# Performance work log

Hardware: AMD Instinct MI355X
Metric: run time of the kernel (lower is better)

The kernel has to match this reference:

```python
import jax, jax.numpy as jnp
import numpy as np

N = 100000
IN_DIM = 512
OUT_DIM = 512


def setup_inputs() -> dict:
    key = jax.random.key(0)
    k1, k2, k3, k4 = jax.random.split(key, 4)
    x = jax.random.normal(k1, (N, IN_DIM), dtype=jnp.float32)
    edge_index = jax.random.randint(k2, (2, N), 0, N, dtype=jnp.int64)
    # Linear params (torch nn.Linear: out = x @ W.T + b)
    bound = 1.0 / np.sqrt(IN_DIM)
    W = jax.random.uniform(k3, (OUT_DIM, IN_DIM), minval=-bound, maxval=bound, dtype=jnp.float32)
    b = jax.random.uniform(k4, (OUT_DIM,), minval=-bound, maxval=bound, dtype=jnp.float32)
    return {"x": x, "edge_index": edge_index, "W": W, "b": b}


def reference(x, edge_index, W, b):
    # out = relu(linear(x))
    out = jax.nn.relu(jnp.einsum('ni,oi->no', x, W) + b)  # [N, OUT_DIM]
    # torch.scatter_add(out, 0, col[:, None], x):
    # index has shape [E, 1] so only column 0 of src (= x) is scattered:
    # out[col[e], 0] += x[e, 0]
    col = edge_index[1].astype(jnp.int32)  # [E], E == N here
    E = col.shape[0]
    out = out.at[col, 0].add(x[:E, 0])
    return out
```

## Files before the change

### kernel.cpp

```cpp
#include <hip/hip_runtime.h>
#include <stdint.h>

#define K_DIM 512
#define N_OUT 512
#define BM 128
#define BN 128
#define BK 64

typedef __bf16 bf16x8 __attribute__((ext_vector_type(8)));
typedef float f32x4 __attribute__((ext_vector_type(4)));
typedef unsigned short ushort8 __attribute__((ext_vector_type(8)));

__device__ inline unsigned short f2bf(float f) {
  unsigned u = __float_as_uint(f);
  u += 0x7fffu + ((u >> 16) & 1u);
  return (unsigned short)(u >> 16);
}

__global__ __launch_bounds__(256) void cvt_bf16_kernel(const float* __restrict__ src,
                                                       unsigned short* __restrict__ dst,
                                                       int n8) {
  int i = blockIdx.x * 256 + threadIdx.x;
  if (i >= n8) return;
  const float4* s = (const float4*)src + (size_t)i * 2;
  float4 a = s[0], c = s[1];
  ushort8 o;
  o[0] = f2bf(a.x); o[1] = f2bf(a.y); o[2] = f2bf(a.z); o[3] = f2bf(a.w);
  o[4] = f2bf(c.x); o[5] = f2bf(c.y); o[6] = f2bf(c.z); o[7] = f2bf(c.w);
  *(ushort8*)(dst + (size_t)i * 8) = o;
}

__global__ __launch_bounds__(256) void gemm_bf16_kernel(
    const unsigned short* __restrict__ xb, const unsigned short* __restrict__ wb,
    const float* __restrict__ b, float* __restrict__ out, int M) {
  __shared__ __align__(16) unsigned short Als[BM * BK];
  __shared__ __align__(16) unsigned short Bls[BN * BK];

  const int tid = threadIdx.x;
  const int lane = tid & 63;
  const int quad = lane >> 4;
  const int l16 = lane & 15;
  const int waveId = tid >> 6;
  const int wm = (waveId >> 1) * 64;
  const int wn = (waveId & 1) * 64;
  const int blockM = blockIdx.y * BM;
  const int blockN = blockIdx.x * BN;

  size_t goffA[4], goffB[4];
  int ldsoff[4];
#pragma unroll
  for (int i = 0; i < 4; ++i) {
    int ch = i * 256 + tid;
    int row = ch >> 3;
    int c8 = ch & 7;
    int sc = c8 ^ (row & 7);
    int ga_row = blockM + row;
    if (ga_row > M - 1) ga_row = M - 1;
    goffA[i] = (size_t)ga_row * K_DIM + sc * 8;
    goffB[i] = (size_t)(blockN + row) * K_DIM + sc * 8;
    ldsoff[i] = ch * 8;
  }

  f32x4 acc[4][4] = {};

  for (int k0 = 0; k0 < K_DIM; k0 += BK) {
#pragma unroll
    for (int i = 0; i < 4; ++i) {
      __builtin_amdgcn_global_load_lds(
          (const __attribute__((address_space(1))) void*)(xb + goffA[i] + k0),
          (__attribute__((address_space(3))) void*)(&Als[ldsoff[i]]), 16, 0, 0);
      __builtin_amdgcn_global_load_lds(
          (const __attribute__((address_space(1))) void*)(wb + goffB[i] + k0),
          (__attribute__((address_space(3))) void*)(&Bls[ldsoff[i]]), 16, 0, 0);
    }
    __syncthreads();

#pragma unroll
    for (int s = 0; s < 2; ++s) {
      bf16x8 af[4], bfr[4];
#pragma unroll
      for (int mi = 0; mi < 4; ++mi) {
        int r = wm + mi * 16 + l16;
        int c = (s * 4 + quad) ^ (r & 7);
        af[mi] = *(const bf16x8*)(&Als[r * BK + c * 8]);
      }
#pragma unroll
      for (int ni = 0; ni < 4; ++ni) {
        int r = wn + ni * 16 + l16;
        int c = (s * 4 + quad) ^ (r & 7);
        bfr[ni] = *(const bf16x8*)(&Bls[r * BK + c * 8]);
      }
#pragma unroll
      for (int mi = 0; mi < 4; ++mi)
#pragma unroll
        for (int ni = 0; ni < 4; ++ni)
          acc[mi][ni] = __builtin_amdgcn_mfma_f32_16x16x32_bf16(af[mi], bfr[ni], acc[mi][ni], 0, 0, 0);
    }
    __syncthreads();
  }

#pragma unroll
  for (int ni = 0; ni < 4; ++ni) {
    int gcol = blockN + wn + ni * 16 + l16;
    float bias = b[gcol];
#pragma unroll
    for (int mi = 0; mi < 4; ++mi) {
#pragma unroll
      for (int r = 0; r < 4; ++r) {
        int grow = blockM + wm + mi * 16 + quad * 4 + r;
        if (grow < M) {
          float v = acc[mi][ni][r] + bias;
          out[(size_t)grow * N_OUT + gcol] = v > 0.f ? v : 0.f;
        }
      }
    }
  }
}

#define LDS_STRIDE 40
__global__ __launch_bounds__(256) void gemm_fused_kernel(
    const float* __restrict__ x, const float* __restrict__ W,
    const float* __restrict__ b, float* __restrict__ out, int M) {
  __shared__ __align__(16) unsigned short Als[BM * LDS_STRIDE];
  __shared__ __align__(16) unsigned short Bls[BN * LDS_STRIDE];
  const int tid = threadIdx.x;
  const int lane = tid & 63;
  const int quad = lane >> 4;
  const int l16 = lane & 15;
  const int waveId = tid >> 6;
  const int wm = (waveId >> 1) * 64;
  const int wn = (waveId & 1) * 64;
  const int blockM = blockIdx.y * BM;
  const int blockN = blockIdx.x * BN;
  f32x4 acc[4][4] = {};
  for (int k0 = 0; k0 < K_DIM; k0 += 32) {
#pragma unroll
    for (int i = 0; i < 4; ++i) {
      int idx = i * 256 + tid;
      int row = idx >> 3;
      int c4 = idx & 7;
      float4 va = make_float4(0.f, 0.f, 0.f, 0.f);
      int grow = blockM + row;
      if (grow < M) va = *(const float4*)(x + (size_t)grow * K_DIM + k0 + c4 * 4);
      ushort4 ha;
      ha.x = f2bf(va.x); ha.y = f2bf(va.y); ha.z = f2bf(va.z); ha.w = f2bf(va.w);
      *(ushort4*)(&Als[row * LDS_STRIDE + c4 * 4]) = ha;
      float4 vb = *(const float4*)(W + (size_t)(blockN + row) * K_DIM + k0 + c4 * 4);
      ushort4 hb;
      hb.x = f2bf(vb.x); hb.y = f2bf(vb.y); hb.z = f2bf(vb.z); hb.w = f2bf(vb.w);
      *(ushort4*)(&Bls[row * LDS_STRIDE + c4 * 4]) = hb;
    }
    __syncthreads();
    bf16x8 af[4], bfr[4];
#pragma unroll
    for (int mi = 0; mi < 4; ++mi)
      af[mi] = *(const bf16x8*)(&Als[(wm + mi * 16 + l16) * LDS_STRIDE + quad * 8]);
#pragma unroll
    for (int ni = 0; ni < 4; ++ni)
      bfr[ni] = *(const bf16x8*)(&Bls[(wn + ni * 16 + l16) * LDS_STRIDE + quad * 8]);
#pragma unroll
    for (int mi = 0; mi < 4; ++mi)
#pragma unroll
      for (int ni = 0; ni < 4; ++ni)
        acc[mi][ni] = __builtin_amdgcn_mfma_f32_16x16x32_bf16(af[mi], bfr[ni], acc[mi][ni], 0, 0, 0);
    __syncthreads();
  }
#pragma unroll
  for (int ni = 0; ni < 4; ++ni) {
    int gcol = blockN + wn + ni * 16 + l16;
    float bias = b[gcol];
#pragma unroll
    for (int mi = 0; mi < 4; ++mi) {
#pragma unroll
      for (int r = 0; r < 4; ++r) {
        int grow = blockM + wm + mi * 16 + quad * 4 + r;
        if (grow < M) {
          float v = acc[mi][ni][r] + bias;
          out[(size_t)grow * N_OUT + gcol] = v > 0.f ? v : 0.f;
        }
      }
    }
  }
}

__global__ void scatter_kernel(const float* __restrict__ x,
                               const int* __restrict__ ei,
                               float* __restrict__ out, int E) {
  int e = blockIdx.x * 256 + threadIdx.x;
  if (e < E) {
    int c = ei[E + e];
    atomicAdd(out + (size_t)c * N_OUT, x[(size_t)e * K_DIM]);
  }
}

extern "C" void kernel_launch(void* const* d_in, const int* in_sizes, int n_in,
                              void* d_out, int out_size, void* d_ws, size_t ws_size,
                              hipStream_t stream) {
  const float* x = (const float*)d_in[0];
  const int* ei = (const int*)d_in[1];
  const float* W = (const float*)d_in[2];
  const float* b = (const float*)d_in[3];
  float* out = (float*)d_out;

  int M = in_sizes[0] / K_DIM;
  int E = in_sizes[1] / 2;

  size_t x_elems = (size_t)M * K_DIM;
  size_t w_elems = (size_t)N_OUT * K_DIM;
  size_t need = (x_elems + w_elems) * 2;

  dim3 grid(N_OUT / BN, (M + BM - 1) / BM);

  if (ws_size >= need) {
    unsigned short* xb = (unsigned short*)d_ws;
    unsigned short* wb = xb + x_elems;
    int n8x = (int)(x_elems / 8);
    int n8w = (int)(w_elems / 8);
    cvt_bf16_kernel<<<(n8x + 255) / 256, 256, 0, stream>>>(x, xb, n8x);
    cvt_bf16_kernel<<<(n8w + 255) / 256, 256, 0, stream>>>(W, wb, n8w);
    gemm_bf16_kernel<<<grid, 256, 0, stream>>>(xb, wb, b, out, M);
  } else {
    gemm_fused_kernel<<<grid, 256, 0, stream>>>(x, W, b, out, M);
  }
  scatter_kernel<<<(E + 255) / 256, 256, 0, stream>>>(x, ei, out, E);
}
```

Before: 496.6 us.

## Fuse x bf16 conversion into GEMM and pre-scatter column zero into buffer

Drops the separate full-matrix fp32-to-bf16 conversion of x. The GEMM now loads fp32 x directly, converts it in registers and writes it to LDS, while W still arrives through the direct global-to-LDS path. The scatter now accumulates into a small per-row buffer that the GEMM epilogue adds to column 0, which removes the atomic read-modify-write pass over the output. The change also adds XCD-aware workgroup remapping and nontemporal output stores. The cost is that the x loads now go through registers, with no async direct-to-LDS copy for A, which adds register pressure and VALU conversion work inside the main loop.

```diff
diff --git a/kernel.cpp b/kernel.cpp
--- a/kernel.cpp
+++ b/kernel.cpp
@@ -30,9 +30,25 @@
   *(ushort8*)(dst + (size_t)i * 8) = o;
 }
 
-__global__ __launch_bounds__(256) void gemm_bf16_kernel(
-    const unsigned short* __restrict__ xb, const unsigned short* __restrict__ wb,
-    const float* __restrict__ b, float* __restrict__ out, int M) {
+__global__ __launch_bounds__(256) void zero_f32_kernel(float* __restrict__ p, int n) {
+  int i = blockIdx.x * 256 + threadIdx.x;
+  if (i < n) p[i] = 0.f;
+}
+
+__global__ __launch_bounds__(256) void scatter_s_kernel(const float* __restrict__ x,
+                                                        const int* __restrict__ ei,
+                                                        float* __restrict__ s, int E) {
+  int e = blockIdx.x * 256 + threadIdx.x;
+  if (e < E) {
+    int c = ei[E + e];
+    atomicAdd(s + c, x[(size_t)e * K_DIM]);
+  }
+}
+
+__global__ __launch_bounds__(256) void gemm_fused2_kernel(
+    const float* __restrict__ x, const unsigned short* __restrict__ wb,
+    const float* __restrict__ b, const float* __restrict__ s,
+    float* __restrict__ out, int M) {
   __shared__ __align__(16) unsigned short Als[BM * BK];
   __shared__ __align__(16) unsigned short Bls[BN * BK];
 
@@ -43,8 +59,14 @@
   const int waveId = tid >> 6;
   const int wm = (waveId >> 1) * 64;
   const int wn = (waveId & 1) * 64;
-  const int blockM = blockIdx.y * BM;
-  const int blockN = blockIdx.x * BN;
+
+  const int nwg = gridDim.x * gridDim.y;
+  int raw = blockIdx.y * gridDim.x + blockIdx.x;
+  int q = nwg >> 3, r = nwg & 7;
+  int xcd = raw & 7;
+  int wg = (xcd < r ? xcd * (q + 1) : r * (q + 1) + (xcd - r) * q) + (raw >> 3);
+  const int blockM = (wg >> 2) * BM;
+  const int blockN = (wg & 3) * BN;
 
   size_t goffA[4], goffB[4];
   int ldsoff[4];
@@ -64,31 +86,41 @@
   f32x4 acc[4][4] = {};
 
   for (int k0 = 0; k0 < K_DIM; k0 += BK) {
-#pragma unroll
-    for (int i = 0; i < 4; ++i) {
-      __builtin_amdgcn_global_load_lds(
-          (const __attribute__((address_space(1))) void*)(xb + goffA[i] + k0),
-          (__attribute__((address_space(3))) void*)(&Als[ldsoff[i]]), 16, 0, 0);
+    float4 a0[4], a1[4];
+#pragma unroll
+    for (int i = 0; i < 4; ++i) {
+      a0[i] = *(const float4*)(x + goffA[i] + k0);
+      a1[i] = *(const float4*)(x + goffA[i] + k0 + 4);
+    }
+#pragma unroll
+    for (int i = 0; i < 4; ++i) {
       __builtin_amdgcn_global_load_lds(
           (const __attribute__((address_space(1))) void*)(wb + goffB[i] + k0),
           (__attribute__((address_space(3))) void*)(&Bls[ldsoff[i]]), 16, 0, 0);
     }
-    __syncthreads();
-
-#pragma unroll
-    for (int s = 0; s < 2; ++s) {
+#pragma unroll
+    for (int i = 0; i < 4; ++i) {
+      ushort8 o;
+      o[0] = f2bf(a0[i].x); o[1] = f2bf(a0[i].y); o[2] = f2bf(a0[i].z); o[3] = f2bf(a0[i].w);
+      o[4] = f2bf(a1[i].x); o[5] = f2bf(a1[i].y); o[6] = f2bf(a1[i].z); o[7] = f2bf(a1[i].w);
+      *(ushort8*)(&Als[ldsoff[i]]) = o;
+    }
+    __syncthreads();
+
+#pragma unroll
+    for (int ss = 0; ss < 2; ++ss) {
       bf16x8 af[4], bfr[4];
 #pragma unroll
       for (int mi = 0; mi < 4; ++mi) {
-        int r = wm + mi * 16 + l16;
-        int c = (s * 4 + quad) ^ (r & 7);
-        af[mi] = *(const bf16x8*)(&Als[r * BK + c * 8]);
+        int rr = wm + mi * 16 + l16;
+        int c = (ss * 4 + quad) ^ (rr & 7);
+        af[mi] = *(const bf16x8*)(&Als[rr * BK + c * 8]);
       }
 #pragma unroll
       for (int ni = 0; ni < 4; ++ni) {
-        int r = wn + ni * 16 + l16;
-        int c = (s * 4 + quad) ^ (r & 7);
-        bfr[ni] = *(const bf16x8*)(&Bls[r * BK + c * 8]);
+        int rr = wn + ni * 16 + l16;
+        int c = (ss * 4 + quad) ^ (rr & 7);
+        bfr[ni] = *(const bf16x8*)(&Bls[rr * BK + c * 8]);
       }
 #pragma unroll
       for (int mi = 0; mi < 4; ++mi)
@@ -106,11 +138,13 @@
 #pragma unroll
     for (int mi = 0; mi < 4; ++mi) {
 #pragma unroll
-      for (int r = 0; r < 4; ++r) {
-        int grow = blockM + wm + mi * 16 + quad * 4 + r;
+      for (int rr = 0; rr < 4; ++rr) {
+        int grow = blockM + wm + mi * 16 + quad * 4 + rr;
         if (grow < M) {
-          float v = acc[mi][ni][r] + bias;
-          out[(size_t)grow * N_OUT + gcol] = v > 0.f ? v : 0.f;
+          float v = acc[mi][ni][rr] + bias;
+          v = v > 0.f ? v : 0.f;
+          if (gcol == 0) v += s[grow];
+          __builtin_nontemporal_store(v, out + (size_t)grow * N_OUT + gcol);
         }
       }
     }
@@ -172,10 +206,10 @@
 #pragma unroll
     for (int mi = 0; mi < 4; ++mi) {
 #pragma unroll
-      for (int r = 0; r < 4; ++r) {
-        int grow = blockM + wm + mi * 16 + quad * 4 + r;
+      for (int rr = 0; rr < 4; ++rr) {
+        int grow = blockM + wm + mi * 16 + quad * 4 + rr;
         if (grow < M) {
-          float v = acc[mi][ni][r] + bias;
+          float v = acc[mi][ni][rr] + bias;
           out[(size_t)grow * N_OUT + gcol] = v > 0.f ? v : 0.f;
         }
       }
@@ -205,22 +239,21 @@
   int M = in_sizes[0] / K_DIM;
   int E = in_sizes[1] / 2;
 
-  size_t x_elems = (size_t)M * K_DIM;
   size_t w_elems = (size_t)N_OUT * K_DIM;
-  size_t need = (x_elems + w_elems) * 2;
+  size_t need = w_elems * 2 + (size_t)M * 4 + 64;
 
   dim3 grid(N_OUT / BN, (M + BM - 1) / BM);
 
   if (ws_size >= need) {
-    unsigned short* xb = (unsigned short*)d_ws;
-    unsigned short* wb = xb + x_elems;
-    int n8x = (int)(x_elems / 8);
+    unsigned short* wb = (unsigned short*)d_ws;
+    float* s = (float*)((char*)d_ws + w_elems * 2);
     int n8w = (int)(w_elems / 8);
-    cvt_bf16_kernel<<<(n8x + 255) / 256, 256, 0, stream>>>(x, xb, n8x);
+    zero_f32_kernel<<<(M + 255) / 256, 256, 0, stream>>>(s, M);
+    scatter_s_kernel<<<(E + 255) / 256, 256, 0, stream>>>(x, ei, s, E);
     cvt_bf16_kernel<<<(n8w + 255) / 256, 256, 0, stream>>>(W, wb, n8w);
-    gemm_bf16_kernel<<<grid, 256, 0, stream>>>(xb, wb, b, out, M);
+    gemm_fused2_kernel<<<grid, 256, 0, stream>>>(x, wb, b, s, out, M);
   } else {
     gemm_fused_kernel<<<grid, 256, 0, stream>>>(x, W, b, out, M);
-  }
-  scatter_kernel<<<(E + 255) / 256, 256, 0, stream>>>(x, ei, out, E);
-}
+    scatter_kernel<<<(E + 255) / 256, 256, 0, stream>>>(x, ei, out, E);
+  }
+}
```

Measured after the change: 478.8 us. 1.04x faster.
